# Kernel tuning notes

Measured on AMD Instinct MI355X. Metric: run time of the kernel, lower is better.

## Reference

```python
import jax, jax.numpy as jnp
import numpy as np

SCALES = [3, 5, 7, 9]


def _conv1d(x, w, b, k):
    # x: (BN, 1, L), w: (1, 1, k), b: (1,) -> (BN, 1, L), 'same' padding (k//2)
    y = jax.lax.conv_general_dilated(
        x, w, window_strides=(1,), padding=[(k // 2, k // 2)],
        dimension_numbers=("NCH", "OIH", "NCH"))
    return y + b[None, :, None]


def setup_inputs() -> dict:
    key = jax.random.key(0)
    ks = jax.random.split(key, 16)
    B, N, L = 64, 321, 720
    inp = {"x": jax.random.normal(ks[0], (B, N, L), dtype=jnp.float32)}
    # Conv1d(1,1,k) params, kaiming-ish scale 1/sqrt(k)
    for i, s in enumerate(SCALES):
        inp[f"cw{i}"] = jax.random.normal(ks[1 + 2 * i], (1, 1, s), dtype=jnp.float32) / np.sqrt(s)
        inp[f"cb{i}"] = jax.random.normal(ks[2 + 2 * i], (1,), dtype=jnp.float32) * 0.01
    # weight_net: Linear(4,32) -> ReLU -> Linear(32,4) -> Softmax
    inp["W1"] = jax.random.normal(ks[10], (4, 32), dtype=jnp.float32) / np.sqrt(4.0)
    inp["b1"] = jnp.zeros((32,), dtype=jnp.float32)
    inp["W2"] = jax.random.normal(ks[11], (32, 4), dtype=jnp.float32) / np.sqrt(32.0)
    inp["b2"] = jnp.zeros((4,), dtype=jnp.float32)
    return inp


def reference(x, cw0, cb0, cw1, cb1, cw2, cb2, cw3, cb3, W1, b1, W2, b2):
    B, N, L = x.shape
    xf = x.reshape(B * N, 1, L)
    cparams = [(cw0, cb0), (cw1, cb1), (cw2, cb2), (cw3, cb3)]
    feats, ents = [], []
    for (w, b), k in zip(cparams, SCALES):
        f = _conv1d(xf, w, b, k)                      # (BN, 1, L)
        prob = jax.nn.softmax(f, axis=-1)
        ent = -(prob * jnp.log(prob + 1e-8)).sum(axis=-1)  # (BN, 1)
        feats.append(f)
        ents.append(ent)
    entropy_vec = jnp.concatenate(ents, axis=-1)      # (BN, 4)
    h = jax.nn.relu(entropy_vec @ W1 + b1)
    weights = jax.nn.softmax(h @ W2 + b2, axis=-1)    # (BN, 4)
    stacked = jnp.stack(feats, axis=1)                # (BN, 4, 1, L)
    trend = (stacked * weights[:, :, None, None]).sum(axis=1)  # (BN, 1, L)
    return trend.reshape(B, N, L)
```

## Files before the change

### kernel.cpp

```cpp
#include <hip/hip_runtime.h>
#include <math.h>

#define NT 256
#define L_LEN 720
#define NROWS (64 * 321)

__global__ __launch_bounds__(NT, 4) void trend_kernel(
    const float* __restrict__ x,
    const float* __restrict__ cw0, const float* __restrict__ cb0,
    const float* __restrict__ cw1, const float* __restrict__ cb1,
    const float* __restrict__ cw2, const float* __restrict__ cb2,
    const float* __restrict__ cw3, const float* __restrict__ cb3,
    const float* __restrict__ W1, const float* __restrict__ b1,
    const float* __restrict__ W2, const float* __restrict__ b2,
    float* __restrict__ out)
{
    const int lane = threadIdx.x & 63;
    const int wid  = threadIdx.x >> 6;
    const int row  = blockIdx.x * 4 + wid;

    const float* __restrict__ xr = x + (size_t)row * L_LEN;

    const float* cws[4] = {cw0, cw1, cw2, cw3};
    const float* cbs[4] = {cb0, cb1, cb2, cb3};
    float w[4][9], bias[4];
#pragma unroll
    for (int s = 0; s < 4; ++s) {
        const int k = 3 + 2 * s;
        bias[s] = cbs[s][0];
#pragma unroll
        for (int t = 0; t < 9; ++t) w[s][t] = (t < k) ? cws[s][t] : 0.0f;
    }

    const bool active = lane < 60;
    float f[4][12];

    if (active) {
        const int e0 = 12 * lane - 4;
        float xw[20];
#pragma unroll
        for (int q = 0; q < 5; ++q) {
            int e = e0 + 4 * q;
            e = (e < 0) ? 0 : ((e > L_LEN - 4) ? (L_LEN - 4) : e);
            float4 v = *(const float4*)(xr + e);
            xw[4 * q + 0] = v.x; xw[4 * q + 1] = v.y;
            xw[4 * q + 2] = v.z; xw[4 * q + 3] = v.w;
        }
        if (lane == 0)  { xw[0] = 0.f; xw[1] = 0.f; xw[2] = 0.f; xw[3] = 0.f; }
        if (lane == 59) { xw[16] = 0.f; xw[17] = 0.f; xw[18] = 0.f; xw[19] = 0.f; }

#pragma unroll
        for (int s = 0; s < 4; ++s) {
            const int k = 3 + 2 * s;
            const int off = 3 - s;
#pragma unroll
            for (int e = 0; e < 12; ++e) {
                float acc = bias[s];
#pragma unroll
                for (int u = 0; u < k; ++u)
                    acc = fmaf(w[s][u], xw[e + off + u], acc);
                f[s][e] = acc;
            }
        }
    } else {
#pragma unroll
        for (int s = 0; s < 4; ++s)
#pragma unroll
            for (int e = 0; e < 12; ++e) f[s][e] = -1e30f;
    }

#pragma unroll
    for (int s = 0; s < 4; ++s)
#pragma unroll
        for (int e = 0; e < 12; ++e)
            asm volatile("" : "+v"(f[s][e]));

    float S[4] = {0.f, 0.f, 0.f, 0.f};
    float T[4] = {0.f, 0.f, 0.f, 0.f};
#pragma unroll
    for (int s = 0; s < 4; ++s) {
#pragma unroll
        for (int e = 0; e < 12; ++e) {
            float g  = f[s][e];
            float ev = __expf(g);
            S[s] += ev;
            T[s] = fmaf(g, ev, T[s]);
        }
    }
#pragma unroll
    for (int s = 0; s < 4; ++s) {
#pragma unroll
        for (int off = 32; off; off >>= 1) {
            S[s] += __shfl_xor(S[s], off);
            T[s] += __shfl_xor(T[s], off);
        }
    }
    float ent[4];
#pragma unroll
    for (int s = 0; s < 4; ++s) ent[s] = __logf(S[s]) - T[s] / S[s];

    const int hidx = lane & 31;
    float h = b1[hidx];
#pragma unroll
    for (int s = 0; s < 4; ++s) h = fmaf(ent[s], W1[s * 32 + hidx], h);
    h = fmaxf(h, 0.0f);

    const float4 w2v = ((const float4*)W2)[hidx];
    float lg[4] = {h * w2v.x, h * w2v.y, h * w2v.z, h * w2v.w};
#pragma unroll
    for (int c = 0; c < 4; ++c) {
#pragma unroll
        for (int off = 16; off; off >>= 1)
            lg[c] += __shfl_xor(lg[c], off);
    }
    lg[0] += b2[0]; lg[1] += b2[1]; lg[2] += b2[2]; lg[3] += b2[3];

    float m = fmaxf(fmaxf(lg[0], lg[1]), fmaxf(lg[2], lg[3]));
    float e0w = __expf(lg[0] - m), e1w = __expf(lg[1] - m);
    float e2w = __expf(lg[2] - m), e3w = __expf(lg[3] - m);
    float inv = 1.0f / (e0w + e1w + e2w + e3w);
    const float w0 = e0w * inv, w1 = e1w * inv, w2 = e2w * inv, w3 = e3w * inv;

    if (active) {
        float* __restrict__ orow = out + (size_t)row * L_LEN + 12 * lane;
#pragma unroll
        for (int q = 0; q < 3; ++q) {
            float4 v;
#pragma unroll
            for (int c = 0; c < 4; ++c) {
                const int e = 4 * q + c;
                float val = w0 * f[0][e];
                val = fmaf(w1, f[1][e], val);
                val = fmaf(w2, f[2][e], val);
                val = fmaf(w3, f[3][e], val);
                ((float*)&v)[c] = val;
            }
            *(float4*)(orow + 4 * q) = v;
        }
    }
}

extern "C" void kernel_launch(void* const* d_in, const int* in_sizes, int n_in,
                              void* d_out, int out_size, void* d_ws, size_t ws_size,
                              hipStream_t stream) {
    const float* xp  = (const float*)d_in[0];
    const float* cw0 = (const float*)d_in[1];
    const float* cb0 = (const float*)d_in[2];
    const float* cw1 = (const float*)d_in[3];
    const float* cb1 = (const float*)d_in[4];
    const float* cw2 = (const float*)d_in[5];
    const float* cb2 = (const float*)d_in[6];
    const float* cw3 = (const float*)d_in[7];
    const float* cb3 = (const float*)d_in[8];
    const float* W1  = (const float*)d_in[9];
    const float* b1  = (const float*)d_in[10];
    const float* W2  = (const float*)d_in[11];
    const float* b2  = (const float*)d_in[12];
    float* outp = (float*)d_out;

    trend_kernel<<<NROWS / 4, NT, 0, stream>>>(xp, cw0, cb0, cw1, cb1, cw2, cb2,
                                               cw3, cb3, W1, b1, W2, b2, outp);
}
```

Baseline: 38.56 us.

## Fold weighted conv features into one merged 9-tap filter and stream entropy sums

Instead of keeping 48 conv outputs per lane in registers, entropy sums are accumulated on the fly in base-2 using hardware exp2/log/rcp builtins. The final trend is then computed by merging the four weighted kernels into a single 9-tap filter applied to the cached input window, recomputing the conv. This cuts register pressure so occupancy can rise (launch bounds raised to 8), at the cost of a second convolution pass and slightly different rounding.

Measured after the change: 39.40 us. +2.2%, slower.

```diff
diff --git a/kernel.cpp b/kernel.cpp
--- a/kernel.cpp
+++ b/kernel.cpp
@@ -5,7 +5,10 @@
 #define L_LEN 720
 #define NROWS (64 * 321)
 
-__global__ __launch_bounds__(NT, 4) void trend_kernel(
+#define LOG2E 1.4426950408889634f
+#define LN2   0.6931471805599453f
+
+__global__ __launch_bounds__(NT, 8) void trend_kernel(
     const float* __restrict__ x,
     const float* __restrict__ cw0, const float* __restrict__ cb0,
     const float* __restrict__ cw1, const float* __restrict__ cb1,
@@ -33,11 +36,13 @@
     }
 
     const bool active = lane < 60;
-    float f[4][12];
+
+    float xw[20];
+    float S[4]  = {0.f, 0.f, 0.f, 0.f};
+    float Tu[4] = {0.f, 0.f, 0.f, 0.f};
 
     if (active) {
         const int e0 = 12 * lane - 4;
-        float xw[20];
 #pragma unroll
         for (int q = 0; q < 5; ++q) {
             int e = e0 + 4 * q;
@@ -50,54 +55,38 @@
         if (lane == 59) { xw[16] = 0.f; xw[17] = 0.f; xw[18] = 0.f; xw[19] = 0.f; }
 
 #pragma unroll
-        for (int s = 0; s < 4; ++s) {
-            const int k = 3 + 2 * s;
-            const int off = 3 - s;
+        for (int e = 0; e < 12; ++e) {
 #pragma unroll
-            for (int e = 0; e < 12; ++e) {
+            for (int s = 0; s < 4; ++s) {
+                const int k = 3 + 2 * s;
+                const int off = 3 - s;
                 float acc = bias[s];
 #pragma unroll
                 for (int u = 0; u < k; ++u)
                     acc = fmaf(w[s][u], xw[e + off + u], acc);
-                f[s][e] = acc;
+                float uu = acc * LOG2E;
+                float ev = __builtin_amdgcn_exp2f(uu);
+                S[s]  += ev;
+                Tu[s]  = fmaf(uu, ev, Tu[s]);
             }
         }
-    } else {
-#pragma unroll
-        for (int s = 0; s < 4; ++s)
-#pragma unroll
-            for (int e = 0; e < 12; ++e) f[s][e] = -1e30f;
     }
 
-#pragma unroll
-    for (int s = 0; s < 4; ++s)
-#pragma unroll
-        for (int e = 0; e < 12; ++e)
-            asm volatile("" : "+v"(f[s][e]));
-
-    float S[4] = {0.f, 0.f, 0.f, 0.f};
-    float T[4] = {0.f, 0.f, 0.f, 0.f};
-#pragma unroll
-    for (int s = 0; s < 4; ++s) {
-#pragma unroll
-        for (int e = 0; e < 12; ++e) {
-            float g  = f[s][e];
-            float ev = __expf(g);
-            S[s] += ev;
-            T[s] = fmaf(g, ev, T[s]);
-        }
-    }
 #pragma unroll
     for (int s = 0; s < 4; ++s) {
 #pragma unroll
         for (int off = 32; off; off >>= 1) {
-            S[s] += __shfl_xor(S[s], off);
-            T[s] += __shfl_xor(T[s], off);
+            S[s]  += __shfl_xor(S[s],  off);
+            Tu[s] += __shfl_xor(Tu[s], off);
         }
     }
+
     float ent[4];
 #pragma unroll
-    for (int s = 0; s < 4; ++s) ent[s] = __logf(S[s]) - T[s] / S[s];
+    for (int s = 0; s < 4; ++s) {
+        float r = __builtin_amdgcn_rcpf(S[s]);
+        ent[s] = LN2 * (__builtin_amdgcn_logf(S[s]) - Tu[s] * r);
+    }
 
     const int hidx = lane & 31;
     float h = b1[hidx];
@@ -119,7 +108,19 @@
     float e0w = __expf(lg[0] - m), e1w = __expf(lg[1] - m);
     float e2w = __expf(lg[2] - m), e3w = __expf(lg[3] - m);
     float inv = 1.0f / (e0w + e1w + e2w + e3w);
-    const float w0 = e0w * inv, w1 = e1w * inv, w2 = e2w * inv, w3 = e3w * inv;
+    const float wgt[4] = {e0w * inv, e1w * inv, e2w * inv, e3w * inv};
+
+    float Wm[9] = {0.f, 0.f, 0.f, 0.f, 0.f, 0.f, 0.f, 0.f, 0.f};
+    float Bm = 0.f;
+#pragma unroll
+    for (int s = 0; s < 4; ++s) {
+        const int k = 3 + 2 * s;
+        const int off = 3 - s;
+#pragma unroll
+        for (int u = 0; u < k; ++u)
+            Wm[off + u] = fmaf(wgt[s], w[s][u], Wm[off + u]);
+        Bm = fmaf(wgt[s], bias[s], Bm);
+    }
 
     if (active) {
         float* __restrict__ orow = out + (size_t)row * L_LEN + 12 * lane;
@@ -129,11 +130,11 @@
 #pragma unroll
             for (int c = 0; c < 4; ++c) {
                 const int e = 4 * q + c;
-                float val = w0 * f[0][e];
-                val = fmaf(w1, f[1][e], val);
-                val = fmaf(w2, f[2][e], val);
-                val = fmaf(w3, f[3][e], val);
-                ((float*)&v)[c] = val;
+                float acc = Bm;
+#pragma unroll
+                for (int j = 0; j < 9; ++j)
+                    acc = fmaf(Wm[j], xw[e + j], acc);
+                ((float*)&v)[c] = acc;
             }
             *(float4*)(orow + 4 * q) = v;
         }
```
